# Kernel optimization log

Measured on AMD Instinct MI355X. Metric: run time of the kernel, lower is better.

Reference implementation:

```python
import jax, jax.numpy as jnp
import numpy as np

IN_DIM, HID_DIM, OUT_DIM, N_EXP = 1024, 4096, 1024, 8
BATCH = 8192


def setup_inputs() -> dict:
    key = jax.random.key(0)
    ks = jax.random.split(key, 8)
    s_in = 1.0 / np.sqrt(IN_DIM)
    s_hid = 1.0 / np.sqrt(HID_DIM)
    return {
        "x": jax.random.normal(ks[0], (BATCH, IN_DIM), jnp.float32),
        "router_w": jax.random.uniform(ks[1], (IN_DIM, N_EXP), jnp.float32, -s_in, s_in),
        "router_b": jax.random.uniform(ks[2], (N_EXP,), jnp.float32, -s_in, s_in),
        "expert_w": jax.random.uniform(ks[3], (N_EXP, IN_DIM, HID_DIM), jnp.float32, -s_in, s_in),
        "expert_b": jax.random.uniform(ks[4], (N_EXP, HID_DIM), jnp.float32, -s_in, s_in),
        "proj_w": jax.random.uniform(ks[5], (HID_DIM, OUT_DIM), jnp.float32, -s_hid, s_hid),
        "proj_b": jax.random.uniform(ks[6], (OUT_DIM,), jnp.float32, -s_hid, s_hid),
    }


def reference(x, router_w, router_b, expert_w, expert_b, proj_w, proj_b):
    # Hard routing: argmax over router logits selects one expert per token.
    logits = x @ router_w + router_b                 # [N, E]
    idx = jnp.argmax(logits, axis=-1)                # [N] int
    n_exp = expert_w.shape[0]
    # Masked per-expert GEMMs (loop over small fixed expert count), summed.
    h = jnp.zeros((x.shape[0], expert_w.shape[2]), dtype=x.dtype)
    for e in range(n_exp):
        mask = (idx == e)[:, None]                   # [N, 1]
        h = h + jnp.where(mask, x @ expert_w[e] + expert_b[e], 0.0)
    out = h @ proj_w + proj_b                        # [N, out_dim]
    routing_weights = jax.nn.one_hot(idx, n_exp, dtype=jnp.float32)
    return out, routing_weights
```

## Files before the change

### kernel.cpp

```cpp
#include <hip/hip_runtime.h>
#include <stdint.h>

#define B_TOK 8192
#define DIN 1024
#define DHID 4096
#define DOUT 1024
#define NE 8

typedef __bf16 bf16x8 __attribute__((ext_vector_type(8)));
typedef float f32x4 __attribute__((ext_vector_type(4)));

__device__ __forceinline__ unsigned short f2bf(float f) {
  union { float f; unsigned u; } v; v.f = f;
  unsigned r = v.u + 0x7fffu + ((v.u >> 16) & 1u);
  return (unsigned short)(r >> 16);
}

__device__ __forceinline__ void async16(const void* g, void* l) {
  __builtin_amdgcn_global_load_lds(
      (__attribute__((address_space(1))) void*)const_cast<void*>(g),
      (__attribute__((address_space(3))) void*)l, 16, 0, 0);
}

__global__ __launch_bounds__(256) void router_kernel(
    const float* __restrict__ x, const float* __restrict__ rw,
    const float* __restrict__ rb, float* __restrict__ oh,
    unsigned short* __restrict__ xb, int* __restrict__ idx,
    int* __restrict__ pos, int* __restrict__ counts)
{
  const int token = blockIdx.x * 4 + (threadIdx.x >> 6);
  const int lane = threadIdx.x & 63;
  const float* xrow = x + (size_t)token * DIN;
  double acc[NE];
#pragma unroll
  for (int e = 0; e < NE; ++e) acc[e] = 0.0;

#pragma unroll
  for (int j = 0; j < 4; ++j) {
    const int v4 = j * 64 + lane;
    const float4 xv = ((const float4*)xrow)[v4];
    const float4* rwr = (const float4*)(rw + (size_t)v4 * 32);
#pragma unroll
    for (int c = 0; c < 4; ++c) {
      const float xs = (&xv.x)[c];
      const float4 w0 = rwr[c * 2 + 0];
      const float4 w1 = rwr[c * 2 + 1];
      acc[0] += (double)(xs * w0.x); acc[1] += (double)(xs * w0.y);
      acc[2] += (double)(xs * w0.z); acc[3] += (double)(xs * w0.w);
      acc[4] += (double)(xs * w1.x); acc[5] += (double)(xs * w1.y);
      acc[6] += (double)(xs * w1.z); acc[7] += (double)(xs * w1.w);
    }
    ushort4 us;
    us.x = f2bf(xv.x); us.y = f2bf(xv.y); us.z = f2bf(xv.z); us.w = f2bf(xv.w);
    ((ushort4*)(xb + (size_t)token * DIN))[v4] = us;
  }
#pragma unroll
  for (int off = 32; off > 0; off >>= 1)
#pragma unroll
    for (int e = 0; e < NE; ++e) acc[e] += __shfl_xor(acc[e], off, 64);

  if (lane == 0) {
    double best = -1e300; int be = 0;
#pragma unroll
    for (int e = 0; e < NE; ++e) {
      const double v = acc[e] + (double)rb[e];
      if (v > best) { best = v; be = e; }
    }
    idx[token] = be;
    pos[token] = atomicAdd(&counts[be], 1);
    float* o = oh + (size_t)token * NE;
#pragma unroll
    for (int e = 0; e < NE; ++e) o[e] = (e == be) ? 1.f : 0.f;
  }
}

__global__ __launch_bounds__(256) void transpose_bf16(
    const float* __restrict__ in, unsigned short* __restrict__ out, int K, int N)
{
  __shared__ float tile[64][65];
  const size_t mat = (size_t)blockIdx.z * (size_t)K * N;
  const int k0 = blockIdx.x * 64, n0 = blockIdx.y * 64;
  const int c = threadIdx.x & 63, r0 = threadIdx.x >> 6;
#pragma unroll
  for (int rr = 0; rr < 64; rr += 4)
    tile[rr + r0][c] = in[mat + (size_t)(k0 + rr + r0) * N + n0 + c];
  __syncthreads();
#pragma unroll
  for (int rr = 0; rr < 64; rr += 4) {
    const int n2 = rr + r0;
    out[mat + (size_t)(n0 + n2) * K + k0 + c] = f2bf(tile[c][n2]);
  }
}

__global__ void slots_kernel(const int* __restrict__ counts, int* __restrict__ offsets,
                             int* __restrict__ slot_e, int* __restrict__ slot_g0,
                             int* __restrict__ slot_nr, int* __restrict__ nslots)
{
  int off = 0, s = 0;
  offsets[0] = 0;
  for (int e = 0; e < NE; ++e) {
    const int c = counts[e];
    for (int t = 0; t < c; t += 128) {
      slot_e[s] = e; slot_g0[s] = off + t;
      slot_nr[s] = (c - t < 128) ? (c - t) : 128;
      ++s;
    }
    off += c;
    offsets[e + 1] = off;
  }
  *nslots = s;
}

__global__ __launch_bounds__(256) void scatter_kernel(
    const int* __restrict__ idx, const int* __restrict__ pos,
    const int* __restrict__ offsets, int* __restrict__ perm)
{
  const int t = blockIdx.x * 256 + threadIdx.x;
  perm[offsets[idx[t]] + pos[t]] = t;
}

__global__ __launch_bounds__(256) void expert_gemm(
    const unsigned short* __restrict__ xb, const unsigned short* __restrict__ Wt,
    const float* __restrict__ eb, const int* __restrict__ perm,
    const int* __restrict__ slot_e, const int* __restrict__ slot_g0,
    const int* __restrict__ slot_nr, const int* __restrict__ nslots,
    unsigned short* __restrict__ h)
{
  const int id = blockIdx.x;
  const int s = id >> 5;
  const int ntile = id & 31;
  if (s >= *nslots) return;
  const int e = slot_e[s];
  const int g0 = slot_g0[s];
  const int nr = slot_nr[s];
  const int n0 = ntile * 128;

  __shared__ __align__(16) unsigned short lsA[2][128 * 64];
  __shared__ __align__(16) unsigned short lsB[2][128 * 64];

  const int tid = threadIdx.x;
  const int w = tid >> 6, lane = tid & 63;
  const int rgrp = lane >> 3, cch = lane & 7;
  const int sw8 = (cch ^ rgrp) * 8;
  const int rowb = w * 32;

  int tok[4];
#pragma unroll
  for (int sub = 0; sub < 4; ++sub) {
    const int row = rowb + sub * 8 + rgrp;
    tok[sub] = perm[g0 + (row < nr ? row : 0)];
  }
  const unsigned short* wb = Wt + (size_t)e * DHID * DIN;

  const f32x4 z = {0.f, 0.f, 0.f, 0.f};
  f32x4 acc[4][4];
#pragma unroll
  for (int i = 0; i < 4; ++i)
#pragma unroll
    for (int j = 0; j < 4; ++j) acc[i][j] = z;

  const int wm = (w & 1) * 64, wn = (w >> 1) * 64;
  const int quad = lane >> 4, l15 = lane & 15;
  int ma[4], nb[4];
#pragma unroll
  for (int i = 0; i < 4; ++i) { ma[i] = wm + i * 16 + l15; nb[i] = wn + i * 16 + l15; }

  auto stage = [&](int bsel, int k0) {
#pragma unroll
    for (int sub = 0; sub < 4; ++sub) {
      const int rbase = rowb + sub * 8;
      async16(xb + (size_t)tok[sub] * DIN + k0 + sw8, &lsA[bsel][rbase * 64]);
      async16(wb + (size_t)(n0 + rbase + rgrp) * DIN + k0 + sw8, &lsB[bsel][rbase * 64]);
    }
  };

  stage(0, 0);
  constexpr int NT = DIN / 64;
  for (int kt = 0; kt < NT; ++kt) {
    const int cur = kt & 1;
    if (kt + 1 < NT) {
      stage(cur ^ 1, (kt + 1) * 64);
      __builtin_amdgcn_sched_barrier(0);
      asm volatile("s_waitcnt vmcnt(8)" ::: "memory");
    } else {
      __builtin_amdgcn_sched_barrier(0);
      asm volatile("s_waitcnt vmcnt(0)" ::: "memory");
    }
    __builtin_amdgcn_sched_barrier(0);
    __builtin_amdgcn_s_barrier();
    __builtin_amdgcn_sched_barrier(0);

#pragma unroll
    for (int ks = 0; ks < 2; ++ks) {
      const int q = ks * 4 + quad;
      bf16x8 af[4], bfr[4];
#pragma unroll
      for (int i = 0; i < 4; ++i)
        af[i] = *(const bf16x8*)&lsA[cur][ma[i] * 64 + ((q ^ (ma[i] & 7)) << 3)];
#pragma unroll
      for (int i = 0; i < 4; ++i)
        bfr[i] = *(const bf16x8*)&lsB[cur][nb[i] * 64 + ((q ^ (nb[i] & 7)) << 3)];
#pragma unroll
      for (int i = 0; i < 4; ++i)
#pragma unroll
        for (int j = 0; j < 4; ++j)
          acc[i][j] = __builtin_amdgcn_mfma_f32_16x16x32_bf16(af[i], bfr[j], acc[i][j], 0, 0, 0);
    }
    __builtin_amdgcn_sched_barrier(0);
    __builtin_amdgcn_s_barrier();
    __builtin_amdgcn_sched_barrier(0);
  }

#pragma unroll
  for (int j = 0; j < 4; ++j) {
    const int col = n0 + nb[j];
    const float bias = eb[e * DHID + col];
#pragma unroll
    for (int i = 0; i < 4; ++i)
#pragma unroll
      for (int r2 = 0; r2 < 4; ++r2) {
        const int row = wm + i * 16 + quad * 4 + r2;
        if (row < nr)
          h[(size_t)(g0 + row) * DHID + col] = f2bf(acc[i][j][r2] + bias);
      }
  }
}

__global__ __launch_bounds__(256) void proj_gemm(
    const unsigned short* __restrict__ hm, const unsigned short* __restrict__ Pt,
    const float* __restrict__ pb, const int* __restrict__ perm,
    float* __restrict__ out)
{
  const int id = blockIdx.x;
  const int m0 = (id & 63) * 128;
  const int n0 = (id >> 6) * 128;
  __shared__ __align__(16) unsigned short lsA[2][128 * 64];
  __shared__ __align__(16) unsigned short lsB[2][128 * 64];

  const int tid = threadIdx.x;
  const int w = tid >> 6, lane = tid & 63;
  const int rgrp = lane >> 3, cch = lane & 7;
  const int sw8 = (cch ^ rgrp) * 8;
  const int rowb = w * 32;

  const f32x4 z = {0.f, 0.f, 0.f, 0.f};
  f32x4 acc[4][4];
#pragma unroll
  for (int i = 0; i < 4; ++i)
#pragma unroll
    for (int j = 0; j < 4; ++j) acc[i][j] = z;

  const int wm = (w & 1) * 64, wn = (w >> 1) * 64;
  const int quad = lane >> 4, l15 = lane & 15;
  int ma[4], nb[4];
#pragma unroll
  for (int i = 0; i < 4; ++i) { ma[i] = wm + i * 16 + l15; nb[i] = wn + i * 16 + l15; }

  auto stage = [&](int bsel, int k0) {
#pragma unroll
    for (int sub = 0; sub < 4; ++sub) {
      const int rbase = rowb + sub * 8;
      async16(hm + (size_t)(m0 + rbase + rgrp) * DHID + k0 + sw8, &lsA[bsel][rbase * 64]);
      async16(Pt + (size_t)(n0 + rbase + rgrp) * DHID + k0 + sw8, &lsB[bsel][rbase * 64]);
    }
  };

  stage(0, 0);
  constexpr int NT = DHID / 64;
  for (int kt = 0; kt < NT; ++kt) {
    const int cur = kt & 1;
    if (kt + 1 < NT) {
      stage(cur ^ 1, (kt + 1) * 64);
      __builtin_amdgcn_sched_barrier(0);
      asm volatile("s_waitcnt vmcnt(8)" ::: "memory");
    } else {
      __builtin_amdgcn_sched_barrier(0);
      asm volatile("s_waitcnt vmcnt(0)" ::: "memory");
    }
    __builtin_amdgcn_sched_barrier(0);
    __builtin_amdgcn_s_barrier();
    __builtin_amdgcn_sched_barrier(0);

#pragma unroll
    for (int ks = 0; ks < 2; ++ks) {
      const int q = ks * 4 + quad;
      bf16x8 af[4], bfr[4];
#pragma unroll
      for (int i = 0; i < 4; ++i)
        af[i] = *(const bf16x8*)&lsA[cur][ma[i] * 64 + ((q ^ (ma[i] & 7)) << 3)];
#pragma unroll
      for (int i = 0; i < 4; ++i)
        bfr[i] = *(const bf16x8*)&lsB[cur][nb[i] * 64 + ((q ^ (nb[i] & 7)) << 3)];
#pragma unroll
      for (int i = 0; i < 4; ++i)
#pragma unroll
        for (int j = 0; j < 4; ++j)
          acc[i][j] = __builtin_amdgcn_mfma_f32_16x16x32_bf16(af[i], bfr[j], acc[i][j], 0, 0, 0);
    }
    __builtin_amdgcn_sched_barrier(0);
    __builtin_amdgcn_s_barrier();
    __builtin_amdgcn_sched_barrier(0);
  }

#pragma unroll
  for (int i = 0; i < 4; ++i)
#pragma unroll
    for (int r2 = 0; r2 < 4; ++r2) {
      const int row = m0 + wm + i * 16 + quad * 4 + r2;
      const int orow = perm[row];
#pragma unroll
      for (int j = 0; j < 4; ++j) {
        const int col = n0 + nb[j];
        out[(size_t)orow * DOUT + col] = acc[i][j][r2] + pb[col];
      }
    }
}

extern "C" void kernel_launch(void* const* d_in, const int* in_sizes, int n_in,
                              void* d_out, int out_size, void* d_ws, size_t ws_size,
                              hipStream_t stream)
{
  const float* x  = (const float*)d_in[0];
  const float* rw = (const float*)d_in[1];
  const float* rb = (const float*)d_in[2];
  const float* ew = (const float*)d_in[3];
  const float* eb = (const float*)d_in[4];
  const float* pw = (const float*)d_in[5];
  const float* pb = (const float*)d_in[6];
  float* out = (float*)d_out;
  float* oh  = out + (size_t)B_TOK * DOUT;

  char* ws = (char*)d_ws;
  constexpr size_t OXB = 0;
  constexpr size_t OWT = OXB + (size_t)B_TOK * DIN * 2;
  constexpr size_t OPT = OWT + (size_t)NE * DHID * DIN * 2;
  constexpr size_t OH  = OPT + (size_t)DOUT * DHID * 2;
  constexpr size_t OIDX = OH + (size_t)B_TOK * DHID * 2;
  constexpr size_t OPOS = OIDX + (size_t)B_TOK * 4;
  constexpr size_t OPRM = OPOS + (size_t)B_TOK * 4;
  constexpr size_t OCNT = OPRM + (size_t)B_TOK * 4;
  constexpr size_t OOFF = OCNT + 256;
  constexpr size_t OSE  = OOFF + 256;
  constexpr size_t OSG  = OSE + 512;
  constexpr size_t OSN  = OSG + 512;
  constexpr size_t ONS  = OSN + 512;
  constexpr size_t NEED = ONS + 512;

  if (ws_size < NEED) {
    hipMemsetAsync(d_out, 0, (size_t)out_size * 4, stream);
    return;
  }

  unsigned short* xb   = (unsigned short*)(ws + OXB);
  unsigned short* Wt   = (unsigned short*)(ws + OWT);
  unsigned short* Pt   = (unsigned short*)(ws + OPT);
  unsigned short* h    = (unsigned short*)(ws + OH);
  int* idx     = (int*)(ws + OIDX);
  int* pos     = (int*)(ws + OPOS);
  int* perm    = (int*)(ws + OPRM);
  int* counts  = (int*)(ws + OCNT);
  int* offsets = (int*)(ws + OOFF);
  int* slot_e  = (int*)(ws + OSE);
  int* slot_g0 = (int*)(ws + OSG);
  int* slot_nr = (int*)(ws + OSN);
  int* nslots  = (int*)(ws + ONS);

  hipMemsetAsync(counts, 0, 64, stream);
  router_kernel<<<B_TOK / 4, 256, 0, stream>>>(x, rw, rb, oh, xb, idx, pos, counts);
  transpose_bf16<<<dim3(DIN / 64, DHID / 64, NE), 256, 0, stream>>>(ew, Wt, DIN, DHID);
  transpose_bf16<<<dim3(DHID / 64, DOUT / 64, 1), 256, 0, stream>>>(pw, Pt, DHID, DOUT);
  slots_kernel<<<1, 1, 0, stream>>>(counts, offsets, slot_e, slot_g0, slot_nr, nslots);
  scatter_kernel<<<B_TOK / 256, 256, 0, stream>>>(idx, pos, offsets, perm);
  expert_gemm<<<72 * 32, 256, 0, stream>>>(
      xb, Wt, eb, perm, slot_e, slot_g0, slot_nr, nslots, h);
  proj_gemm<<<(B_TOK / 128) * (DOUT / 128), 256, 0, stream>>>(h, Pt, pb, perm, out);
}
```

Measured before the change: 588.5 us.

## Enlarge GEMM tiles to 256x128 with 8 waves and split-phase prefetch schedule

Both the expert and projection GEMMs move from 128x128 tiles on 4 waves to 256x128 tiles on 8 waves (512 threads), and expert slots grow to 256 tokens. The main loop is restructured into two half-K phases: part of the next tile's loads is issued before the barrier and the rest interleaved after the LDS reads, with setprio raised around the MFMA bursts. The aim is better operand reuse per LDS byte and more overlap of global loads with MFMA work. In exchange it uses more LDS per block and has fewer blocks in flight, and padding waste in the last partial slot of each expert grows.

```diff
diff --git a/kernel.cpp b/kernel.cpp
--- a/kernel.cpp
+++ b/kernel.cpp
@@ -100,9 +100,9 @@
   offsets[0] = 0;
   for (int e = 0; e < NE; ++e) {
     const int c = counts[e];
-    for (int t = 0; t < c; t += 128) {
+    for (int t = 0; t < c; t += 256) {
       slot_e[s] = e; slot_g0[s] = off + t;
-      slot_nr[s] = (c - t < 128) ? (c - t) : 128;
+      slot_nr[s] = (c - t < 256) ? (c - t) : 256;
       ++s;
     }
     off += c;
@@ -119,7 +119,7 @@
   perm[offsets[idx[t]] + pos[t]] = t;
 }
 
-__global__ __launch_bounds__(256) void expert_gemm(
+__global__ __launch_bounds__(512) void expert_gemm(
     const unsigned short* __restrict__ xb, const unsigned short* __restrict__ Wt,
     const float* __restrict__ eb, const int* __restrict__ perm,
     const int* __restrict__ slot_e, const int* __restrict__ slot_g0,
@@ -135,182 +135,212 @@
   const int nr = slot_nr[s];
   const int n0 = ntile * 128;
 
-  __shared__ __align__(16) unsigned short lsA[2][128 * 64];
+  __shared__ __align__(16) unsigned short lsA[2][256 * 64];
   __shared__ __align__(16) unsigned short lsB[2][128 * 64];
 
   const int tid = threadIdx.x;
   const int w = tid >> 6, lane = tid & 63;
   const int rgrp = lane >> 3, cch = lane & 7;
   const int sw8 = (cch ^ rgrp) * 8;
-  const int rowb = w * 32;
-
-  int tok[4];
-#pragma unroll
-  for (int sub = 0; sub < 4; ++sub) {
-    const int row = rowb + sub * 8 + rgrp;
-    tok[sub] = perm[g0 + (row < nr ? row : 0)];
-  }
-  const unsigned short* wb = Wt + (size_t)e * DHID * DIN;
-
+  const int wr = w >> 2, wc = w & 3;
+  const int quad = lane >> 4, l15 = lane & 15;
+
+  const unsigned short* ap[4];
+#pragma unroll
+  for (int hh = 0; hh < 2; ++hh)
+#pragma unroll
+    for (int l = 0; l < 2; ++l) {
+      const int row = hh * 128 + l * 64 + w * 8 + rgrp;
+      ap[hh * 2 + l] = xb + (size_t)perm[g0 + (row < nr ? row : 0)] * DIN + sw8;
+    }
+  const unsigned short* wbp = Wt + (size_t)e * DHID * DIN;
+  const unsigned short* bp[2];
+#pragma unroll
+  for (int hh = 0; hh < 2; ++hh)
+    bp[hh] = wbp + (size_t)(n0 + hh * 64 + w * 8 + rgrp) * DIN + sw8;
+
+  f32x4 acc[8][2];
   const f32x4 z = {0.f, 0.f, 0.f, 0.f};
-  f32x4 acc[4][4];
-#pragma unroll
-  for (int i = 0; i < 4; ++i)
-#pragma unroll
-    for (int j = 0; j < 4; ++j) acc[i][j] = z;
-
-  const int wm = (w & 1) * 64, wn = (w >> 1) * 64;
-  const int quad = lane >> 4, l15 = lane & 15;
-  int ma[4], nb[4];
-#pragma unroll
-  for (int i = 0; i < 4; ++i) { ma[i] = wm + i * 16 + l15; nb[i] = wn + i * 16 + l15; }
-
-  auto stage = [&](int bsel, int k0) {
-#pragma unroll
-    for (int sub = 0; sub < 4; ++sub) {
-      const int rbase = rowb + sub * 8;
-      async16(xb + (size_t)tok[sub] * DIN + k0 + sw8, &lsA[bsel][rbase * 64]);
-      async16(wb + (size_t)(n0 + rbase + rgrp) * DIN + k0 + sw8, &lsB[bsel][rbase * 64]);
-    }
-  };
-
-  stage(0, 0);
+#pragma unroll
+  for (int i = 0; i < 8; ++i) { acc[i][0] = z; acc[i][1] = z; }
+
+  auto stageA0 = [&](int db, int k0) {
+    async16(ap[0] + k0, &lsA[db][(w * 8) * 64]);
+    async16(ap[1] + k0, &lsA[db][(64 + w * 8) * 64]);
+  };
+  auto stageRest = [&](int db, int k0) {
+    async16(ap[2] + k0, &lsA[db][(128 + w * 8) * 64]);
+    async16(ap[3] + k0, &lsA[db][(192 + w * 8) * 64]);
+    async16(bp[0] + k0, &lsB[db][(w * 8) * 64]);
+    async16(bp[1] + k0, &lsB[db][(64 + w * 8) * 64]);
+  };
+
+  auto phase = [&](int db, int ks, bool dostage, int k0n) {
+    bf16x8 af[8], bfv[2];
+    const int q = ks * 4 + quad;
+#pragma unroll
+    for (int i = 0; i < 8; ++i) {
+      const int row = wr * 128 + i * 16 + l15;
+      af[i] = *(const bf16x8*)&lsA[db][row * 64 + ((q ^ (row & 7)) << 3)];
+    }
+#pragma unroll
+    for (int j = 0; j < 2; ++j) {
+      const int row = wc * 32 + j * 16 + l15;
+      bfv[j] = *(const bf16x8*)&lsB[db][row * 64 + ((q ^ (row & 7)) << 3)];
+    }
+    if (dostage) stageRest(db ^ 1, k0n);
+    __builtin_amdgcn_s_barrier();
+    asm volatile("s_waitcnt lgkmcnt(0)" ::: "memory");
+    __builtin_amdgcn_sched_barrier(0);
+    __builtin_amdgcn_s_setprio(1);
+#pragma unroll
+    for (int i = 0; i < 8; ++i)
+#pragma unroll
+      for (int j = 0; j < 2; ++j)
+        acc[i][j] = __builtin_amdgcn_mfma_f32_16x16x32_bf16(af[i], bfv[j], acc[i][j], 0, 0, 0);
+    __builtin_amdgcn_s_setprio(0);
+    __builtin_amdgcn_s_barrier();
+  };
+
+  auto tile = [&](int db, int t, bool notlast) {
+    if (notlast) {
+      stageA0(db ^ 1, (t + 1) * 64);
+      asm volatile("s_waitcnt vmcnt(2)" ::: "memory");
+    } else {
+      asm volatile("s_waitcnt vmcnt(0)" ::: "memory");
+    }
+    __builtin_amdgcn_s_barrier();
+    phase(db, 0, notlast, (t + 1) * 64);
+    phase(db, 1, false, 0);
+  };
+
+  stageA0(0, 0);
+  stageRest(0, 0);
   constexpr int NT = DIN / 64;
-  for (int kt = 0; kt < NT; ++kt) {
-    const int cur = kt & 1;
-    if (kt + 1 < NT) {
-      stage(cur ^ 1, (kt + 1) * 64);
-      __builtin_amdgcn_sched_barrier(0);
-      asm volatile("s_waitcnt vmcnt(8)" ::: "memory");
-    } else {
-      __builtin_amdgcn_sched_barrier(0);
-      asm volatile("s_waitcnt vmcnt(0)" ::: "memory");
-    }
-    __builtin_amdgcn_sched_barrier(0);
-    __builtin_amdgcn_s_barrier();
-    __builtin_amdgcn_sched_barrier(0);
-
-#pragma unroll
-    for (int ks = 0; ks < 2; ++ks) {
-      const int q = ks * 4 + quad;
-      bf16x8 af[4], bfr[4];
-#pragma unroll
-      for (int i = 0; i < 4; ++i)
-        af[i] = *(const bf16x8*)&lsA[cur][ma[i] * 64 + ((q ^ (ma[i] & 7)) << 3)];
-#pragma unroll
-      for (int i = 0; i < 4; ++i)
-        bfr[i] = *(const bf16x8*)&lsB[cur][nb[i] * 64 + ((q ^ (nb[i] & 7)) << 3)];
-#pragma unroll
-      for (int i = 0; i < 4; ++i)
-#pragma unroll
-        for (int j = 0; j < 4; ++j)
-          acc[i][j] = __builtin_amdgcn_mfma_f32_16x16x32_bf16(af[i], bfr[j], acc[i][j], 0, 0, 0);
-    }
-    __builtin_amdgcn_sched_barrier(0);
-    __builtin_amdgcn_s_barrier();
-    __builtin_amdgcn_sched_barrier(0);
-  }
-
-#pragma unroll
-  for (int j = 0; j < 4; ++j) {
-    const int col = n0 + nb[j];
+  for (int t = 0; t < NT; t += 2) {
+    tile(0, t, true);
+    tile(1, t + 1, t + 2 < NT);
+  }
+
+#pragma unroll
+  for (int j = 0; j < 2; ++j) {
+    const int col = n0 + wc * 32 + j * 16 + l15;
     const float bias = eb[e * DHID + col];
 #pragma unroll
-    for (int i = 0; i < 4; ++i)
+    for (int i = 0; i < 8; ++i)
 #pragma unroll
       for (int r2 = 0; r2 < 4; ++r2) {
-        const int row = wm + i * 16 + quad * 4 + r2;
+        const int row = wr * 128 + i * 16 + quad * 4 + r2;
         if (row < nr)
           h[(size_t)(g0 + row) * DHID + col] = f2bf(acc[i][j][r2] + bias);
       }
   }
 }
 
-__global__ __launch_bounds__(256) void proj_gemm(
+__global__ __launch_bounds__(512) void proj_gemm(
     const unsigned short* __restrict__ hm, const unsigned short* __restrict__ Pt,
     const float* __restrict__ pb, const int* __restrict__ perm,
     float* __restrict__ out)
 {
   const int id = blockIdx.x;
-  const int m0 = (id & 63) * 128;
-  const int n0 = (id >> 6) * 128;
-  __shared__ __align__(16) unsigned short lsA[2][128 * 64];
+  const int m0 = (id & 31) * 256;
+  const int n0 = (id >> 5) * 128;
+
+  __shared__ __align__(16) unsigned short lsA[2][256 * 64];
   __shared__ __align__(16) unsigned short lsB[2][128 * 64];
 
   const int tid = threadIdx.x;
   const int w = tid >> 6, lane = tid & 63;
   const int rgrp = lane >> 3, cch = lane & 7;
   const int sw8 = (cch ^ rgrp) * 8;
-  const int rowb = w * 32;
-
+  const int wr = w >> 2, wc = w & 3;
+  const int quad = lane >> 4, l15 = lane & 15;
+
+  const unsigned short* ap[4];
+#pragma unroll
+  for (int hh = 0; hh < 2; ++hh)
+#pragma unroll
+    for (int l = 0; l < 2; ++l) {
+      const int row = m0 + hh * 128 + l * 64 + w * 8 + rgrp;
+      ap[hh * 2 + l] = hm + (size_t)row * DHID + sw8;
+    }
+  const unsigned short* bp[2];
+#pragma unroll
+  for (int hh = 0; hh < 2; ++hh)
+    bp[hh] = Pt + (size_t)(n0 + hh * 64 + w * 8 + rgrp) * DHID + sw8;
+
+  f32x4 acc[8][2];
   const f32x4 z = {0.f, 0.f, 0.f, 0.f};
-  f32x4 acc[4][4];
-#pragma unroll
-  for (int i = 0; i < 4; ++i)
-#pragma unroll
-    for (int j = 0; j < 4; ++j) acc[i][j] = z;
-
-  const int wm = (w & 1) * 64, wn = (w >> 1) * 64;
-  const int quad = lane >> 4, l15 = lane & 15;
-  int ma[4], nb[4];
-#pragma unroll
-  for (int i = 0; i < 4; ++i) { ma[i] = wm + i * 16 + l15; nb[i] = wn + i * 16 + l15; }
-
-  auto stage = [&](int bsel, int k0) {
-#pragma unroll
-    for (int sub = 0; sub < 4; ++sub) {
-      const int rbase = rowb + sub * 8;
-      async16(hm + (size_t)(m0 + rbase + rgrp) * DHID + k0 + sw8, &lsA[bsel][rbase * 64]);
-      async16(Pt + (size_t)(n0 + rbase + rgrp) * DHID + k0 + sw8, &lsB[bsel][rbase * 64]);
-    }
-  };
-
-  stage(0, 0);
+#pragma unroll
+  for (int i = 0; i < 8; ++i) { acc[i][0] = z; acc[i][1] = z; }
+
+  auto stageA0 = [&](int db, int k0) {
+    async16(ap[0] + k0, &lsA[db][(w * 8) * 64]);
+    async16(ap[1] + k0, &lsA[db][(64 + w * 8) * 64]);
+  };
+  auto stageRest = [&](int db, int k0) {
+    async16(ap[2] + k0, &lsA[db][(128 + w * 8) * 64]);
+    async16(ap[3] + k0, &lsA[db][(192 + w * 8) * 64]);
+    async16(bp[0] + k0, &lsB[db][(w * 8) * 64]);
+    async16(bp[1] + k0, &lsB[db][(64 + w * 8) * 64]);
+  };
+
+  auto phase = [&](int db, int ks, bool dostage, int k0n) {
+    bf16x8 af[8], bfv[2];
+    const int q = ks * 4 + quad;
+#pragma unroll
+    for (int i = 0; i < 8; ++i) {
+      const int row = wr * 128 + i * 16 + l15;
+      af[i] = *(const bf16x8*)&lsA[db][row * 64 + ((q ^ (row & 7)) << 3)];
+    }
+#pragma unroll
+    for (int j = 0; j < 2; ++j) {
+      const int row = wc * 32 + j * 16 + l15;
+      bfv[j] = *(const bf16x8*)&lsB[db][row * 64 + ((q ^ (row & 7)) << 3)];
+    }
+    if (dostage) stageRest(db ^ 1, k0n);
+    __builtin_amdgcn_s_barrier();
+    asm volatile("s_waitcnt lgkmcnt(0)" ::: "memory");
+    __builtin_amdgcn_sched_barrier(0);
+    __builtin_amdgcn_s_setprio(1);
+#pragma unroll
+    for (int i = 0; i < 8; ++i)
+#pragma unroll
+      for (int j = 0; j < 2; ++j)
+        acc[i][j] = __builtin_amdgcn_mfma_f32_16x16x32_bf16(af[i], bfv[j], acc[i][j], 0, 0, 0);
+    __builtin_amdgcn_s_setprio(0);
+    __builtin_amdgcn_s_barrier();
+  };
+
+  auto tile = [&](int db, int t, bool notlast) {
+    if (notlast) {
+      stageA0(db ^ 1, (t + 1) * 64);
+      asm volatile("s_waitcnt vmcnt(2)" ::: "memory");
+    } else {
+      asm volatile("s_waitcnt vmcnt(0)" ::: "memory");
+    }
+    __builtin_amdgcn_s_barrier();
+    phase(db, 0, notlast, (t + 1) * 64);
+    phase(db, 1, false, 0);
+  };
+
+  stageA0(0, 0);
+  stageRest(0, 0);
   constexpr int NT = DHID / 64;
-  for (int kt = 0; kt < NT; ++kt) {
-    const int cur = kt & 1;
-    if (kt + 1 < NT) {
-      stage(cur ^ 1, (kt + 1) * 64);
-      __builtin_amdgcn_sched_barrier(0);
-      asm volatile("s_waitcnt vmcnt(8)" ::: "memory");
-    } else {
-      __builtin_amdgcn_sched_barrier(0);
-      asm volatile("s_waitcnt vmcnt(0)" ::: "memory");
-    }
-    __builtin_amdgcn_sched_barrier(0);
-    __builtin_amdgcn_s_barrier();
-    __builtin_amdgcn_sched_barrier(0);
-
-#pragma unroll
-    for (int ks = 0; ks < 2; ++ks) {
-      const int q = ks * 4 + quad;
-      bf16x8 af[4], bfr[4];
-#pragma unroll
-      for (int i = 0; i < 4; ++i)
-        af[i] = *(const bf16x8*)&lsA[cur][ma[i] * 64 + ((q ^ (ma[i] & 7)) << 3)];
-#pragma unroll
-      for (int i = 0; i < 4; ++i)
-        bfr[i] = *(const bf16x8*)&lsB[cur][nb[i] * 64 + ((q ^ (nb[i] & 7)) << 3)];
-#pragma unroll
-      for (int i = 0; i < 4; ++i)
-#pragma unroll
-        for (int j = 0; j < 4; ++j)
-          acc[i][j] = __builtin_amdgcn_mfma_f32_16x16x32_bf16(af[i], bfr[j], acc[i][j], 0, 0, 0);
-    }
-    __builtin_amdgcn_sched_barrier(0);
-    __builtin_amdgcn_s_barrier();
-    __builtin_amdgcn_sched_barrier(0);
-  }
-
-#pragma unroll
-  for (int i = 0; i < 4; ++i)
+  for (int t = 0; t < NT; t += 2) {
+    tile(0, t, true);
+    tile(1, t + 1, t + 2 < NT);
+  }
+
+#pragma unroll
+  for (int i = 0; i < 8; ++i)
 #pragma unroll
     for (int r2 = 0; r2 < 4; ++r2) {
-      const int row = m0 + wm + i * 16 + quad * 4 + r2;
+      const int row = m0 + wr * 128 + i * 16 + quad * 4 + r2;
       const int orow = perm[row];
 #pragma unroll
-      for (int j = 0; j < 4; ++j) {
-        const int col = n0 + nb[j];
+      for (int j = 0; j < 2; ++j) {
+        const int col = n0 + wc * 32 + j * 16 + l15;
         out[(size_t)orow * DOUT + col] = acc[i][j][r2] + pb[col];
       }
     }
@@ -371,7 +401,7 @@
   transpose_bf16<<<dim3(DHID / 64, DOUT / 64, 1), 256, 0, stream>>>(pw, Pt, DHID, DOUT);
   slots_kernel<<<1, 1, 0, stream>>>(counts, offsets, slot_e, slot_g0, slot_nr, nslots);
   scatter_kernel<<<B_TOK / 256, 256, 0, stream>>>(idx, pos, offsets, perm);
-  expert_gemm<<<72 * 32, 256, 0, stream>>>(
+  expert_gemm<<<40 * 32, 512, 0, stream>>>(
       xb, Wt, eb, perm, slot_e, slot_g0, slot_nr, nslots, h);
-  proj_gemm<<<(B_TOK / 128) * (DOUT / 128), 256, 0, stream>>>(h, Pt, pb, perm, out);
-}
+  proj_gemm<<<(DOUT / 128) * (B_TOK / 256), 512, 0, stream>>>(h, Pt, pb, perm, out);
+}
```

After: 603.3 us. 1.03x slower.
